# Kernel tuning notes

Measured on AMD Instinct MI355X. Metric: run time of the kernel, lower is better.

The kernel has to match this reference:

```python
import jax, jax.numpy as jnp
import numpy as np

SEQ_LEN = 4096
HIDDEN = 1280
NUM_HEADS = 16
HEAD_DIM = HIDDEN // NUM_HEADS  # 80
NUM_SEQS = 8


def setup_inputs() -> dict:
    key = jax.random.key(0)
    ks = jax.random.split(key, 8)
    x = jax.random.normal(ks[0], (SEQ_LEN, HIDDEN), dtype=jnp.float32)
    # rotary tables: use cos/sin of random angles so they are bounded like real RoPE tables
    ang = jax.random.uniform(ks[1], (SEQ_LEN, HEAD_DIM), dtype=jnp.float32) * 6.283185
    cos = jnp.cos(ang)
    sin = jnp.sin(ang)
    # variable-length packed segments: strictly increasing boundaries incl. 0 and SEQ_LEN
    rng = np.random.default_rng(0)
    inner = np.sort(rng.choice(np.arange(1, SEQ_LEN), size=NUM_SEQS - 1, replace=False))
    cu_seqlens = jnp.asarray(np.concatenate([[0], inner, [SEQ_LEN]]), dtype=jnp.int32)
    s = 0.02
    w_qkv = jax.random.normal(ks[2], (HIDDEN, 3 * HIDDEN), dtype=jnp.float32) * s
    b_qkv = jnp.zeros((3 * HIDDEN,), dtype=jnp.float32)
    w_proj = jax.random.normal(ks[3], (HIDDEN, HIDDEN), dtype=jnp.float32) * s
    b_proj = jnp.zeros((HIDDEN,), dtype=jnp.float32)
    return {"x": x, "cu_seqlens": cu_seqlens, "cos": cos, "sin": sin,
            "w_qkv": w_qkv, "b_qkv": b_qkv, "w_proj": w_proj, "b_proj": b_proj}


def _rotate_half(t):
    d = t.shape[-1] // 2
    return jnp.concatenate([-t[..., d:], t[..., :d]], axis=-1)


def _apply_rope(q, k, cos, sin):
    # q,k: (S,H,D); cos,sin: (S,D) broadcast over heads, computed in fp32
    c = cos[:, None, :].astype(jnp.float32)
    s = sin[:, None, :].astype(jnp.float32)
    qf, kf = q.astype(jnp.float32), k.astype(jnp.float32)
    q_out = qf * c + _rotate_half(qf) * s
    k_out = kf * c + _rotate_half(kf) * s
    return q_out.astype(q.dtype), k_out.astype(k.dtype)


def reference(x, cu_seqlens, cos, sin, w_qkv, b_qkv, w_proj, b_proj):
    S = x.shape[0]
    scale = HEAD_DIM ** (-0.5)
    qkv = (x @ w_qkv + b_qkv).reshape(S, 3, NUM_HEADS, HEAD_DIM)
    q, k, v = qkv[:, 0], qkv[:, 1], qkv[:, 2]  # each (S,H,D)
    q, k = _apply_rope(q, k, cos, sin)
    # block-diagonal varlen attention via segment-id mask (same math as per-chunk softmax)
    pos = jnp.arange(S)
    seg = jnp.searchsorted(cu_seqlens[1:], pos, side='right')  # (S,) segment id
    mask = seg[:, None] == seg[None, :]  # (S,S) block-diagonal
    scores = jnp.einsum('shd,thd->hst', q, k) * scale  # (H,S,S)
    scores = jnp.where(mask[None], scores.astype(jnp.float32), jnp.finfo(jnp.float32).min)
    attn = jax.nn.softmax(scores, axis=-1).astype(q.dtype)
    out = jnp.einsum('hst,thd->shd', attn, v).reshape(S, NUM_HEADS * HEAD_DIM)
    return out @ w_proj + b_proj
```

## Files before the change

### kernel.cpp

```cpp
#include <hip/hip_runtime.h>
#include <cstdint>
#include <cstddef>

typedef __bf16 bf16x8 __attribute__((ext_vector_type(8)));
typedef float f32x4 __attribute__((ext_vector_type(4)));
typedef float f32x16 __attribute__((ext_vector_type(16)));
typedef unsigned short u16x8 __attribute__((ext_vector_type(8)));

#define SEQ   4096
#define HID   1280
#define NH    16
#define HD    80

__device__ __forceinline__ unsigned short f2bf(float f) {
  unsigned int u = __float_as_uint(f);
  unsigned int r = u + 0x7FFFu + ((u >> 16) & 1u);
  return (unsigned short)(r >> 16);
}
__device__ __forceinline__ float bf2f(unsigned short h) {
  return __uint_as_float(((unsigned int)h) << 16);
}
__device__ __forceinline__ __bf16 us2bf(unsigned short u) {
  union { unsigned short s; __bf16 b; } c; c.s = u; return c.b;
}
__device__ __forceinline__ void dma16(const void* g, void* l) {
  __builtin_amdgcn_global_load_lds((const __attribute__((address_space(1))) unsigned int*)g,
                                   (__attribute__((address_space(3))) unsigned int*)l, 16, 0, 0);
}
__device__ __forceinline__ unsigned int cvtpk(float a, float b) {
  unsigned int w;
  asm("v_cvt_pk_bf16_f32 %0, %1, %2" : "=v"(w) : "v"(a), "v"(b));
  return w;
}
__device__ __forceinline__ float lo2f(unsigned int w) { return __uint_as_float(w << 16); }
__device__ __forceinline__ float hi2f(unsigned int w) { return __uint_as_float(w & 0xffff0000u); }

__global__ __launch_bounds__(256) void split_hi_kernel(const float* __restrict__ x,
                                                       unsigned short* __restrict__ hi,
                                                       int n4) {
  int i = blockIdx.x * 256 + threadIdx.x;
  if (i >= n4) return;
  float4 v = *((const float4*)x + i);
  *((ushort4*)hi + i) = make_ushort4(f2bf(v.x), f2bf(v.y), f2bf(v.z), f2bf(v.w));
}

__global__ __launch_bounds__(256) void tsplit_kernel(const float* __restrict__ W,
                                                     unsigned short* __restrict__ Thi,
                                                     unsigned short* __restrict__ Tlo,
                                                     int K, int N) {
  __shared__ float tile[32][33];
  int n0 = blockIdx.x * 32, k0 = blockIdx.y * 32;
  int tx = threadIdx.x & 31, ty = threadIdx.x >> 5;
#pragma unroll
  for (int i = 0; i < 32; i += 8)
    tile[ty + i][tx] = W[(size_t)(k0 + ty + i) * N + n0 + tx];
  __syncthreads();
#pragma unroll
  for (int i = 0; i < 32; i += 8) {
    float v = tile[tx][ty + i];
    size_t idx = (size_t)(n0 + ty + i) * K + (size_t)(k0 + tx);
    unsigned short h = f2bf(v);
    Thi[idx] = h;
    Tlo[idx] = f2bf(v - bf2f(h));
  }
}

__global__ __launch_bounds__(256, 3) void gemm128_x2(
    const unsigned short* __restrict__ A, const unsigned short* __restrict__ Bh,
    const unsigned short* __restrict__ Bl, const float* __restrict__ bias,
    float* __restrict__ out0, float* __restrict__ out1, float* __restrict__ out2,
    int M, int N, int K) {
  __shared__ __align__(16) unsigned short sALL[3 * 8192];

  const int t = threadIdx.x;
  const int lane = t & 63, wave = t >> 6;
  const int c16 = lane & 15, quad = lane >> 4;
  const int bm = blockIdx.y * 128, bn = blockIdx.x * 128;
  const int wr = (wave >> 1) * 64, wc = (wave & 1) * 64;
  const int lrow = lane >> 3;
  const int lswz = (lane & 7) ^ lrow;

  f32x4 acc[4][4];
#pragma unroll
  for (int i = 0; i < 4; ++i)
#pragma unroll
    for (int j = 0; j < 4; ++j) acc[i][j] = (f32x4){0.f, 0.f, 0.f, 0.f};

  const unsigned short* gp[12];
#pragma unroll
  for (int i = 0; i < 12; ++i) {
    const int ua = wave * 12 + i;
    const int arr = ua >> 4, sub = ua & 15;
    const unsigned short* g = (arr == 0) ? A : (arr == 1) ? Bh : Bl;
    const int rowg = ((arr == 0) ? bm : bn) + sub * 8 + lrow;
    gp[i] = g + (size_t)rowg * K + lswz * 8;
  }

  for (int k0 = 0; k0 < K; k0 += 64) {
    __syncthreads();
#pragma unroll
    for (int i = 0; i < 12; ++i)
      dma16(gp[i] + k0, &sALL[(wave * 12 + i) * 512]);
    __syncthreads();
#pragma unroll
    for (int ks = 0; ks < 2; ++ks) {
      bf16x8 a[4], bh[4], bl[4];
#pragma unroll
      for (int mi = 0; mi < 4; ++mi) {
        const int row = wr + mi * 16 + c16;
        const int off = row * 64 + (((ks * 4 + quad) ^ (row & 7)) * 8);
        a[mi] = *(const bf16x8*)&sALL[off];
      }
#pragma unroll
      for (int ni = 0; ni < 4; ++ni) {
        const int row = wc + ni * 16 + c16;
        const int off = row * 64 + (((ks * 4 + quad) ^ (row & 7)) * 8);
        bh[ni] = *(const bf16x8*)&sALL[8192 + off];
        bl[ni] = *(const bf16x8*)&sALL[16384 + off];
      }
#pragma unroll
      for (int mi = 0; mi < 4; ++mi)
#pragma unroll
        for (int ni = 0; ni < 4; ++ni) {
          acc[mi][ni] = __builtin_amdgcn_mfma_f32_16x16x32_bf16(a[mi], bh[ni], acc[mi][ni], 0, 0, 0);
          acc[mi][ni] = __builtin_amdgcn_mfma_f32_16x16x32_bf16(a[mi], bl[ni], acc[mi][ni], 0, 0, 0);
        }
    }
  }
#pragma unroll
  for (int ni = 0; ni < 4; ++ni) {
    int colg = bn + wc + ni * 16 + c16;
    float bv = bias[colg];
    float* op;
    int c = colg;
    if (c < 1280) op = out0;
    else if (c < 2560) { op = out1; c -= 1280; }
    else { op = out2; c -= 2560; }
#pragma unroll
    for (int mi = 0; mi < 4; ++mi)
#pragma unroll
      for (int r = 0; r < 4; ++r) {
        int rowg = bm + wr + mi * 16 + quad * 4 + r;
        op[(size_t)rowg * 1280 + c] = acc[mi][ni][r] + bv;
      }
  }
}

__global__ __launch_bounds__(256) void rope_pack_kernel(
    float* __restrict__ qf, const float* __restrict__ kf,
    const float* __restrict__ cs, const float* __restrict__ sn,
    unsigned short* __restrict__ khi, unsigned short* __restrict__ klo) {
  const int h = blockIdx.y;
  const int s = blockIdx.x * 64 + (threadIdx.x >> 2);
  const int p = threadIdx.x & 3;
  float* qrow = qf + (size_t)s * HID + h * HD;
  const float* krow = kf + (size_t)s * HID + h * HD;
  const float* cr = cs + (size_t)s * HD;
  const float* sr = sn + (size_t)s * HD;
  unsigned short* kh = khi + ((size_t)h * SEQ + s) * HD;
  unsigned short* kl = klo + ((size_t)h * SEQ + s) * HD;
#pragma unroll
  for (int j = 0; j < 10; ++j) {
    int d = 10 * p + j;
    float c0 = cr[d], s0 = sr[d], c1 = cr[d + 40], s1 = sr[d + 40];
    float q0 = qrow[d], q1 = qrow[d + 40];
    qrow[d]      = q0 * c0 - q1 * s0;
    qrow[d + 40] = q1 * c1 + q0 * s1;
    float k0 = krow[d], k1 = krow[d + 40];
    float kn0 = k0 * c0 - k1 * s0;
    float kn1 = k1 * c1 + k0 * s1;
    unsigned short h0 = f2bf(kn0), h1 = f2bf(kn1);
    kh[d] = h0;      kl[d] = f2bf(kn0 - bf2f(h0));
    kh[d + 40] = h1; kl[d + 40] = f2bf(kn1 - bf2f(h1));
  }
}

__global__ __launch_bounds__(256) void vt_pack_kernel(const float* __restrict__ vf,
                                                      unsigned short* __restrict__ vthi,
                                                      unsigned short* __restrict__ vtlo) {
  __shared__ unsigned short sTh[80][72];
  __shared__ unsigned short sTl[80][72];
  const int h = blockIdx.y;
  const int s0 = blockIdx.x * 64;
  const int t = threadIdx.x;
  {
    int row = t >> 2, p = (t & 3) * 20;
    const float* src = vf + (size_t)(s0 + row) * HID + h * HD + p;
#pragma unroll
    for (int i = 0; i < 5; ++i) {
      float4 v = *(const float4*)(src + 4 * i);
      float vv[4] = {v.x, v.y, v.z, v.w};
#pragma unroll
      for (int j = 0; j < 4; ++j) {
        int d = p + 4 * i + j;
        unsigned short hu = f2bf(vv[j]);
        sTh[d][row] = hu;
        sTl[d][row] = f2bf(vv[j] - bf2f(hu));
      }
    }
  }
  __syncthreads();
  if (t < 160) {
    int d = t >> 1, half = (t & 1) * 32;
    size_t base = (size_t)(h * HD + d) * SEQ + s0 + half;
#pragma unroll
    for (int i = 0; i < 8; ++i) {
      *(ushort4*)&vthi[base + 4 * i] = *(ushort4*)&sTh[d][half + 4 * i];
      *(ushort4*)&vtlo[base + 4 * i] = *(ushort4*)&sTl[d][half + 4 * i];
    }
  }
}


#define MFMA32(A, B, C) __builtin_amdgcn_mfma_f32_32x32x16_bf16(A, B, C, 0, 0, 0)

__global__ __launch_bounds__(128, 2) void attn_kernel(
    const float* __restrict__ qf, const unsigned short* __restrict__ khi,
    const unsigned short* __restrict__ klo, const unsigned short* __restrict__ vthi,
    const unsigned short* __restrict__ vtlo, const int* __restrict__ cu,
    unsigned short* __restrict__ ohi) {
  __shared__ __align__(16) unsigned short sAll[20480];
  unsigned short* const sKh = sAll;
  unsigned short* const sKl = sAll + 5120;
  unsigned short* const sVh = sAll + 10240;
  unsigned short* const sVl = sAll + 15360;

  const int t = threadIdx.x;
  const int lane = t & 63, wave = t >> 6;
  const int ln5 = lane & 31;
  const int hi  = lane >> 5;
  const int ln7 = lane & 7;
  const int lr8 = lane >> 3;
  const int vswz = (lane & 7) ^ lr8;

  const unsigned int u = (blockIdx.x & 7) * 128 + (blockIdx.x >> 3);
  const int h = (int)(u >> 6);
  const int r0 = (int)(u & 63u) * 64;

  int cu_r[9];
#pragma unroll
  for (int i = 0; i < 9; ++i) cu_r[i] = cu[i];

  const int q_my = r0 + wave * 32 + ln5;
  int sq = 0, sg0 = 0, sg1 = 0;
#pragma unroll
  for (int i = 1; i < 8; ++i) {
    sq  += (q_my    >= cu_r[i]) ? 1 : 0;
    sg0 += (r0      >= cu_r[i]) ? 1 : 0;
    sg1 += (r0 + 63 >= cu_r[i]) ? 1 : 0;
  }
  const int kb_lo = cu_r[sq], kb_hi = cu_r[sq + 1];
  const int ck0 = cu_r[sg0] & ~63;
  const int kend = cu_r[sg1 + 1];
  const int nchunk = (kend - ck0 + 63) >> 6;

  int ccol[5];
#pragma unroll
  for (int c = 0; c < 5; ++c)
    ccol[c] = (c < 4) ? ((((2 * c) + hi) ^ ln7) * 8) : ((8 + hi) * 8);

  int koff[10];
#pragma unroll
  for (int i = 0; i < 10; ++i) {
    const int G = i * 64 + lane;
    const int key = (G * 205) >> 11;
    const int p = G - key * 10;
    const int cl = (p < 8) ? (p ^ (key & 7)) : p;
    koff[i] = key * 80 + cl * 8;
  }

  const float qsc = 0.11180339887498949f;
  bf16x8 qh[5], ql[5];
  {
    const float* qrow = qf + (size_t)q_my * HID + h * HD;
#pragma unroll
    for (int kt = 0; kt < 5; ++kt) {
      const int d0 = kt * 16 + hi * 8;
      float4 a0 = *(const float4*)(qrow + d0);
      float4 a1 = *(const float4*)(qrow + d0 + 4);
      float va[8] = {a0.x, a0.y, a0.z, a0.w, a1.x, a1.y, a1.z, a1.w};
      bf16x8 hf, lf;
#pragma unroll
      for (int j = 0; j < 8; ++j) {
        float v = va[j] * qsc;
        unsigned short hu = f2bf(v);
        hf[j] = us2bf(hu);
        lf[j] = us2bf(f2bf(v - bf2f(hu)));
      }
      qh[kt] = hf; ql[kt] = lf;
    }
  }

  f32x16 O0, O1, O2;
#pragma unroll
  for (int r = 0; r < 16; ++r) { O0[r] = 0.f; O1[r] = 0.f; O2[r] = 0.f; }
  float m_i = -1e30f, l_i = 0.f;

  auto STAGE_K = [&](int ck) {
    const unsigned short* gk = (wave & 1) ? klo : khi;
    unsigned short* lk = (wave & 1) ? sKl : sKh;
    const unsigned short* gb = gk + ((size_t)h * SEQ + ck) * 80;
#pragma unroll
    for (int i2 = 0; i2 < 10; ++i2) dma16(gb + koff[i2], lk + i2 * 512);
  };
  auto STAGE_V = [&](int ck) {
    const unsigned short* gv = (wave & 1) ? vtlo : vthi;
    unsigned short* lv = (wave & 1) ? sVl : sVh;
#pragma unroll
    for (int i2 = 0; i2 < 10; ++i2)
      dma16(gv + (size_t)(h * HD + 8 * i2 + lr8) * SEQ + ck + vswz * 8, lv + i2 * 512);
  };

  STAGE_K(ck0);
  STAGE_V(ck0);
  __syncthreads();

  for (int ci = 0; ci < nchunk; ++ci) {
    const int ck = ck0 + ci * 64;

    f32x16 sc0, sc1;
#pragma unroll
    for (int r = 0; r < 16; ++r) { sc0[r] = 0.f; sc1[r] = 0.f; }
    __builtin_amdgcn_s_setprio(1);
#pragma unroll
    for (int kd = 0; kd < 5; ++kd) {
      const int col = ccol[kd];
      bf16x8 kha = *(const bf16x8*)&sKh[ln5 * 80 + col];
      bf16x8 kla = *(const bf16x8*)&sKl[ln5 * 80 + col];
      bf16x8 khb = *(const bf16x8*)&sKh[(32 + ln5) * 80 + col];
      bf16x8 klb = *(const bf16x8*)&sKl[(32 + ln5) * 80 + col];
      sc0 = MFMA32(kha, qh[kd], sc0); sc1 = MFMA32(khb, qh[kd], sc1);
      sc0 = MFMA32(kha, ql[kd], sc0); sc1 = MFMA32(khb, ql[kd], sc1);
      sc0 = MFMA32(kla, qh[kd], sc0); sc1 = MFMA32(klb, qh[kd], sc1);
    }
    __builtin_amdgcn_s_setprio(0);

    float mx = -1e30f;
#define MSK(SCV, KT2)                                                          \
    {                                                                          \
      const int kb = ck + (KT2) * 32 + 4 * hi;                                 \
      _Pragma("unroll")                                                        \
      for (int r = 0; r < 16; ++r) {                                           \
        const int kg = kb + (r & 3) + 8 * (r >> 2);                            \
        float v = (kg >= kb_lo && kg < kb_hi) ? SCV[r] : -1e30f;               \
        SCV[r] = v;                                                            \
        mx = fmaxf(mx, v);                                                     \
      }                                                                        \
    }
    MSK(sc0, 0)
    MSK(sc1, 1)
#undef MSK
    mx = fmaxf(mx, __shfl_xor(mx, 32));
    const float mnew = fmaxf(m_i, mx);
    const float alpha = __expf(m_i - mnew);
    float ps = 0.f;
#define EXPP(SCV)                                                              \
    _Pragma("unroll")                                                          \
    for (int r = 0; r < 16; ++r) {                                             \
      const float s = SCV[r];                                                  \
      const float p = (s > -1e29f) ? __expf(s - mnew) : 0.f;                   \
      ps += p;                                                                 \
      SCV[r] = p;                                                              \
    }
    EXPP(sc0)
    EXPP(sc1)
#undef EXPP
    ps += __shfl_xor(ps, 32);
    l_i = l_i * alpha + ps;
    m_i = mnew;
#pragma unroll
    for (int r = 0; r < 16; ++r) { O0[r] *= alpha; O1[r] *= alpha; O2[r] *= alpha; }

    __syncthreads();
    if (ci + 1 < nchunk) STAGE_K(ck + 64);

    __builtin_amdgcn_s_setprio(1);
#define PV_STEP(SCV, SUB, KT)                                                  \
    {                                                                          \
      unsigned int A1 = cvtpk(SCV[(SUB)*8+0], SCV[(SUB)*8+1]);                 \
      unsigned int A2 = cvtpk(SCV[(SUB)*8+2], SCV[(SUB)*8+3]);                 \
      unsigned int B1 = cvtpk(SCV[(SUB)*8+4], SCV[(SUB)*8+5]);                 \
      unsigned int B2 = cvtpk(SCV[(SUB)*8+6], SCV[(SUB)*8+7]);                 \
      float e0 = SCV[(SUB)*8+0] - lo2f(A1), e1 = SCV[(SUB)*8+1] - hi2f(A1);    \
      float e2 = SCV[(SUB)*8+2] - lo2f(A2), e3 = SCV[(SUB)*8+3] - hi2f(A2);    \
      float e4 = SCV[(SUB)*8+4] - lo2f(B1), e5 = SCV[(SUB)*8+5] - hi2f(B1);    \
      float e6 = SCV[(SUB)*8+6] - lo2f(B2), e7 = SCV[(SUB)*8+7] - hi2f(B2);    \
      unsigned int C1 = cvtpk(e0, e1), C2 = cvtpk(e2, e3);                     \
      unsigned int D1 = cvtpk(e4, e5), D2 = cvtpk(e6, e7);                     \
      unsigned int T1 = (unsigned int)__shfl_xor((int)(hi ? A1 : B1), 32);     \
      unsigned int T2 = (unsigned int)__shfl_xor((int)(hi ? A2 : B2), 32);     \
      unsigned int U1 = (unsigned int)__shfl_xor((int)(hi ? C1 : D1), 32);     \
      unsigned int U2 = (unsigned int)__shfl_xor((int)(hi ? C2 : D2), 32);     \
      union { unsigned int w[4]; bf16x8 v; } ph_, pl_;                         \
      ph_.w[0] = hi ? T1 : A1;  ph_.w[1] = hi ? T2 : A2;                       \
      ph_.w[2] = hi ? B1 : T1;  ph_.w[3] = hi ? B2 : T2;                       \
      pl_.w[0] = hi ? U1 : C1;  pl_.w[1] = hi ? U2 : C2;                       \
      pl_.w[2] = hi ? D1 : U1;  pl_.w[3] = hi ? D2 : U2;                       \
      const int vc = ccol[KT];                                                 \
      bf16x8 vh0 = *(const bf16x8*)&sVh[ln5 * 64 + vc];                        \
      bf16x8 vh1 = *(const bf16x8*)&sVh[(32 + ln5) * 64 + vc];                 \
      bf16x8 vh2 = *(const bf16x8*)&sVh[(64 + (ln5 & 15)) * 64 + vc];          \
      bf16x8 vl0 = *(const bf16x8*)&sVl[ln5 * 64 + vc];                        \
      bf16x8 vl1 = *(const bf16x8*)&sVl[(32 + ln5) * 64 + vc];                 \
      bf16x8 vl2 = *(const bf16x8*)&sVl[(64 + (ln5 & 15)) * 64 + vc];          \
      O0 = MFMA32(vh0, ph_.v, O0); O1 = MFMA32(vh1, ph_.v, O1);                \
      O2 = MFMA32(vh2, ph_.v, O2);                                             \
      O0 = MFMA32(vl0, ph_.v, O0); O1 = MFMA32(vl1, ph_.v, O1);                \
      O2 = MFMA32(vl2, ph_.v, O2);                                             \
      O0 = MFMA32(vh0, pl_.v, O0); O1 = MFMA32(vh1, pl_.v, O1);                \
      O2 = MFMA32(vh2, pl_.v, O2);                                             \
    }
    PV_STEP(sc0, 0, 0)
    PV_STEP(sc0, 1, 1)
    PV_STEP(sc1, 0, 2)
    PV_STEP(sc1, 1, 3)
#undef PV_STEP
    __builtin_amdgcn_s_setprio(0);

    __syncthreads();
    if (ci + 1 < nchunk) STAGE_V(ck + 64);
  }

  const float inv = 1.0f / l_i;
  unsigned short* tr = sAll + wave * 3072;
#define WR(OV, DT)                                                             \
  _Pragma("unroll")                                                            \
  for (int r = 0; r < 16; r += 2) {                                            \
    if ((DT) < 2 || r < 8) {                                                   \
      const int d = (DT) * 32 + (r & 3) + 8 * (r >> 2) + 4 * hi;               \
      unsigned int w = cvtpk(OV[r] * inv, OV[r + 1] * inv);                    \
      *(unsigned int*)&tr[ln5 * 96 + d] = w;                                   \
    }                                                                          \
  }
  WR(O0, 0)
  WR(O1, 1)
  WR(O2, 2)
#undef WR
  __syncthreads();
  {
    const int qq = lane >> 1, part = lane & 1;
    const unsigned short* src = tr + qq * 96 + part * 40;
    unsigned short* dst = ohi + (size_t)(r0 + wave * 32 + qq) * HID + h * HD + part * 40;
#pragma unroll
    for (int i = 0; i < 5; ++i)
      *(u16x8*)&dst[i * 8] = *(const u16x8*)&src[i * 8];
  }
}

extern "C" void kernel_launch(void* const* d_in, const int* in_sizes, int n_in,
                              void* d_out, int out_size, void* d_ws, size_t ws_size,
                              hipStream_t stream) {
  const float* x      = (const float*)d_in[0];
  const int*   cu     = (const int*)d_in[1];
  const float* cs     = (const float*)d_in[2];
  const float* sn     = (const float*)d_in[3];
  const float* w_qkv  = (const float*)d_in[4];
  const float* b_qkv  = (const float*)d_in[5];
  const float* w_proj = (const float*)d_in[6];
  const float* b_proj = (const float*)d_in[7];
  float* out = (float*)d_out;

  char* ws = (char*)d_ws;
  float*          qf     = (float*)(ws + 0);
  float*          kf     = (float*)(ws + 20971520ULL);
  unsigned short* vthi   = (unsigned short*)(ws + 20971520ULL);
  unsigned short* vtlo   = (unsigned short*)(ws + 31457280ULL);
  float*          vf     = (float*)(ws + 41943040ULL);
  unsigned short* o_hi   = (unsigned short*)(ws + 41943040ULL);
  unsigned short* x_hi   = (unsigned short*)(ws + 62914560ULL);
  unsigned short* khi    = (unsigned short*)(ws + 62914560ULL);
  unsigned short* klo    = (unsigned short*)(ws + 73400320ULL);
  unsigned short* wqt_hi = (unsigned short*)(ws + 83886080ULL);
  unsigned short* wqt_lo = (unsigned short*)(ws + 93716480ULL);
  unsigned short* wpt_hi = (unsigned short*)(ws + 103546880ULL);
  unsigned short* wpt_lo = (unsigned short*)(ws + 106823680ULL);

  split_hi_kernel<<<5120, 256, 0, stream>>>(x, x_hi, 1310720);
  tsplit_kernel<<<dim3(120, 40), 256, 0, stream>>>(w_qkv, wqt_hi, wqt_lo, 1280, 3840);
  tsplit_kernel<<<dim3(40, 40), 256, 0, stream>>>(w_proj, wpt_hi, wpt_lo, 1280, 1280);
  gemm128_x2<<<dim3(30, 32), 256, 0, stream>>>(x_hi, wqt_hi, wqt_lo, b_qkv,
                                               qf, kf, vf, 4096, 3840, 1280);
  rope_pack_kernel<<<dim3(64, 16), 256, 0, stream>>>(qf, kf, cs, sn, khi, klo);
  vt_pack_kernel<<<dim3(64, 16), 256, 0, stream>>>(vf, vthi, vtlo);
  attn_kernel<<<1024, 128, 0, stream>>>(qf, khi, klo, vthi, vtlo, cu, o_hi);
  gemm128_x2<<<dim3(10, 32), 256, 0, stream>>>(o_hi, wpt_hi, wpt_lo, b_proj,
                                               out, nullptr, nullptr, 4096, 1280, 1280);
}
```

Baseline: 369.0 us.

## Persistent per-wave attention with longest-first work queue and 32-key chunks

The attention kernel becomes persistent. Each wave independently pulls 32-query tiles from an atomic counter, in an order computed by a new single-block scheduler that sorts tiles by key-chunk count, longest first. Each wave gets its own LDS buffers and streams 32-key chunks using vmcnt-based waits instead of block-wide barriers. Scores are pre-scaled by log2(e) so exp2f replaces __expf, and the output is written straight from registers without the LDS transpose. The aim is to cut load imbalance from the varlen segments and the barrier stalls, at the cost of an extra kernel launch, atomics, and smaller MFMA tiles per chunk.

```diff
diff --git a/kernel.cpp b/kernel.cpp
--- a/kernel.cpp
+++ b/kernel.cpp
@@ -5,7 +5,6 @@
 typedef __bf16 bf16x8 __attribute__((ext_vector_type(8)));
 typedef float f32x4 __attribute__((ext_vector_type(4)));
 typedef float f32x16 __attribute__((ext_vector_type(16)));
-typedef unsigned short u16x8 __attribute__((ext_vector_type(8)));
 
 #define SEQ   4096
 #define HID   1280
@@ -211,6 +210,35 @@
   }
 }
 
+__global__ __launch_bounds__(128) void sched_kernel(const int* __restrict__ cu,
+                                                    int* __restrict__ perm,
+                                                    unsigned int* __restrict__ ctr) {
+  __shared__ int w[128];
+  const int t = threadIdx.x;
+  if (t == 0) *ctr = 0u;
+  int cu_r[9];
+#pragma unroll
+  for (int i = 0; i < 9; ++i) cu_r[i] = cu[i];
+  const int r0 = t * 32;
+  int sg0 = 0, sg1 = 0;
+#pragma unroll
+  for (int i = 1; i < 8; ++i) {
+    sg0 += (r0      >= cu_r[i]) ? 1 : 0;
+    sg1 += (r0 + 31 >= cu_r[i]) ? 1 : 0;
+  }
+  const int ck0 = cu_r[sg0] & ~31;
+  const int kend = cu_r[sg1 + 1];
+  w[t] = (kend - ck0 + 31) >> 5;
+  __syncthreads();
+  const int wt = w[t];
+  int rank = 0;
+  for (int i = 0; i < 128; ++i)
+    rank += ((w[i] > wt) || (w[i] == wt && i < t)) ? 1 : 0;
+#pragma unroll
+  for (int hh = 0; hh < 16; ++hh)
+    perm[rank * 16 + hh] = hh * 128 + t;
+}
+
 
 #define MFMA32(A, B, C) __builtin_amdgcn_mfma_f32_32x32x16_bf16(A, B, C, 0, 0, 0)
 
@@ -218,232 +246,252 @@
     const float* __restrict__ qf, const unsigned short* __restrict__ khi,
     const unsigned short* __restrict__ klo, const unsigned short* __restrict__ vthi,
     const unsigned short* __restrict__ vtlo, const int* __restrict__ cu,
-    unsigned short* __restrict__ ohi) {
+    unsigned short* __restrict__ ohi, const int* __restrict__ perm,
+    unsigned int* __restrict__ ctr) {
   __shared__ __align__(16) unsigned short sAll[20480];
-  unsigned short* const sKh = sAll;
-  unsigned short* const sKl = sAll + 5120;
-  unsigned short* const sVh = sAll + 10240;
-  unsigned short* const sVl = sAll + 15360;
 
   const int t = threadIdx.x;
   const int lane = t & 63, wave = t >> 6;
   const int ln5 = lane & 31;
   const int hi  = lane >> 5;
   const int ln7 = lane & 7;
-  const int lr8 = lane >> 3;
-  const int vswz = (lane & 7) ^ lr8;
-
-  const unsigned int u = (blockIdx.x & 7) * 128 + (blockIdx.x >> 3);
-  const int h = (int)(u >> 6);
-  const int r0 = (int)(u & 63u) * 64;
+
+  unsigned short* const wb  = sAll + wave * 10240;
+  unsigned short* const sKh = wb;
+  unsigned short* const sKl = wb + 2560;
+  unsigned short* const sVh = wb + 5120;
+  unsigned short* const sVl = wb + 7680;
 
   int cu_r[9];
 #pragma unroll
   for (int i = 0; i < 9; ++i) cu_r[i] = cu[i];
 
-  const int q_my = r0 + wave * 32 + ln5;
-  int sq = 0, sg0 = 0, sg1 = 0;
-#pragma unroll
-  for (int i = 1; i < 8; ++i) {
-    sq  += (q_my    >= cu_r[i]) ? 1 : 0;
-    sg0 += (r0      >= cu_r[i]) ? 1 : 0;
-    sg1 += (r0 + 63 >= cu_r[i]) ? 1 : 0;
-  }
-  const int kb_lo = cu_r[sq], kb_hi = cu_r[sq + 1];
-  const int ck0 = cu_r[sg0] & ~63;
-  const int kend = cu_r[sg1 + 1];
-  const int nchunk = (kend - ck0 + 63) >> 6;
-
-  int ccol[5];
-#pragma unroll
-  for (int c = 0; c < 5; ++c)
-    ccol[c] = (c < 4) ? ((((2 * c) + hi) ^ ln7) * 8) : ((8 + hi) * 8);
-
-  int koff[10];
-#pragma unroll
-  for (int i = 0; i < 10; ++i) {
+  int koff[5];
+#pragma unroll
+  for (int i = 0; i < 5; ++i) {
     const int G = i * 64 + lane;
     const int key = (G * 205) >> 11;
     const int p = G - key * 10;
     const int cl = (p < 8) ? (p ^ (key & 7)) : p;
     koff[i] = key * 80 + cl * 8;
   }
-
-  const float qsc = 0.11180339887498949f;
-  bf16x8 qh[5], ql[5];
-  {
-    const float* qrow = qf + (size_t)q_my * HID + h * HD;
-#pragma unroll
-    for (int kt = 0; kt < 5; ++kt) {
-      const int d0 = kt * 16 + hi * 8;
-      float4 a0 = *(const float4*)(qrow + d0);
-      float4 a1 = *(const float4*)(qrow + d0 + 4);
-      float va[8] = {a0.x, a0.y, a0.z, a0.w, a1.x, a1.y, a1.z, a1.w};
-      bf16x8 hf, lf;
-#pragma unroll
-      for (int j = 0; j < 8; ++j) {
-        float v = va[j] * qsc;
-        unsigned short hu = f2bf(v);
-        hf[j] = us2bf(hu);
-        lf[j] = us2bf(f2bf(v - bf2f(hu)));
-      }
-      qh[kt] = hf; ql[kt] = lf;
-    }
-  }
-
-  f32x16 O0, O1, O2;
-#pragma unroll
-  for (int r = 0; r < 16; ++r) { O0[r] = 0.f; O1[r] = 0.f; O2[r] = 0.f; }
-  float m_i = -1e30f, l_i = 0.f;
-
-  auto STAGE_K = [&](int ck) {
-    const unsigned short* gk = (wave & 1) ? klo : khi;
-    unsigned short* lk = (wave & 1) ? sKl : sKh;
-    const unsigned short* gb = gk + ((size_t)h * SEQ + ck) * 80;
-#pragma unroll
-    for (int i2 = 0; i2 < 10; ++i2) dma16(gb + koff[i2], lk + i2 * 512);
-  };
-  auto STAGE_V = [&](int ck) {
-    const unsigned short* gv = (wave & 1) ? vtlo : vthi;
-    unsigned short* lv = (wave & 1) ? sVl : sVh;
-#pragma unroll
-    for (int i2 = 0; i2 < 10; ++i2)
-      dma16(gv + (size_t)(h * HD + 8 * i2 + lr8) * SEQ + ck + vswz * 8, lv + i2 * 512);
-  };
-
-  STAGE_K(ck0);
-  STAGE_V(ck0);
-  __syncthreads();
-
-  for (int ci = 0; ci < nchunk; ++ci) {
-    const int ck = ck0 + ci * 64;
-
-    f32x16 sc0, sc1;
-#pragma unroll
-    for (int r = 0; r < 16; ++r) { sc0[r] = 0.f; sc1[r] = 0.f; }
-    __builtin_amdgcn_s_setprio(1);
-#pragma unroll
-    for (int kd = 0; kd < 5; ++kd) {
-      const int col = ccol[kd];
-      bf16x8 kha = *(const bf16x8*)&sKh[ln5 * 80 + col];
-      bf16x8 kla = *(const bf16x8*)&sKl[ln5 * 80 + col];
-      bf16x8 khb = *(const bf16x8*)&sKh[(32 + ln5) * 80 + col];
-      bf16x8 klb = *(const bf16x8*)&sKl[(32 + ln5) * 80 + col];
-      sc0 = MFMA32(kha, qh[kd], sc0); sc1 = MFMA32(khb, qh[kd], sc1);
-      sc0 = MFMA32(kha, ql[kd], sc0); sc1 = MFMA32(khb, ql[kd], sc1);
-      sc0 = MFMA32(kla, qh[kd], sc0); sc1 = MFMA32(klb, qh[kd], sc1);
-    }
-    __builtin_amdgcn_s_setprio(0);
-
-    float mx = -1e30f;
-#define MSK(SCV, KT2)                                                          \
-    {                                                                          \
-      const int kb = ck + (KT2) * 32 + 4 * hi;                                 \
-      _Pragma("unroll")                                                        \
-      for (int r = 0; r < 16; ++r) {                                           \
-        const int kg = kb + (r & 3) + 8 * (r >> 2);                            \
-        float v = (kg >= kb_lo && kg < kb_hi) ? SCV[r] : -1e30f;               \
-        SCV[r] = v;                                                            \
-        mx = fmaxf(mx, v);                                                     \
-      }                                                                        \
-    }
-    MSK(sc0, 0)
-    MSK(sc1, 1)
-#undef MSK
-    mx = fmaxf(mx, __shfl_xor(mx, 32));
-    const float mnew = fmaxf(m_i, mx);
-    const float alpha = __expf(m_i - mnew);
-    float ps = 0.f;
-#define EXPP(SCV)                                                              \
-    _Pragma("unroll")                                                          \
-    for (int r = 0; r < 16; ++r) {                                             \
-      const float s = SCV[r];                                                  \
-      const float p = (s > -1e29f) ? __expf(s - mnew) : 0.f;                   \
-      ps += p;                                                                 \
-      SCV[r] = p;                                                              \
-    }
-    EXPP(sc0)
-    EXPP(sc1)
-#undef EXPP
-    ps += __shfl_xor(ps, 32);
-    l_i = l_i * alpha + ps;
-    m_i = mnew;
-#pragma unroll
-    for (int r = 0; r < 16; ++r) { O0[r] *= alpha; O1[r] *= alpha; O2[r] *= alpha; }
-
-    __syncthreads();
-    if (ci + 1 < nchunk) STAGE_K(ck + 64);
-
-    __builtin_amdgcn_s_setprio(1);
-#define PV_STEP(SCV, SUB, KT)                                                  \
-    {                                                                          \
-      unsigned int A1 = cvtpk(SCV[(SUB)*8+0], SCV[(SUB)*8+1]);                 \
-      unsigned int A2 = cvtpk(SCV[(SUB)*8+2], SCV[(SUB)*8+3]);                 \
-      unsigned int B1 = cvtpk(SCV[(SUB)*8+4], SCV[(SUB)*8+5]);                 \
-      unsigned int B2 = cvtpk(SCV[(SUB)*8+6], SCV[(SUB)*8+7]);                 \
-      float e0 = SCV[(SUB)*8+0] - lo2f(A1), e1 = SCV[(SUB)*8+1] - hi2f(A1);    \
-      float e2 = SCV[(SUB)*8+2] - lo2f(A2), e3 = SCV[(SUB)*8+3] - hi2f(A2);    \
-      float e4 = SCV[(SUB)*8+4] - lo2f(B1), e5 = SCV[(SUB)*8+5] - hi2f(B1);    \
-      float e6 = SCV[(SUB)*8+6] - lo2f(B2), e7 = SCV[(SUB)*8+7] - hi2f(B2);    \
-      unsigned int C1 = cvtpk(e0, e1), C2 = cvtpk(e2, e3);                     \
-      unsigned int D1 = cvtpk(e4, e5), D2 = cvtpk(e6, e7);                     \
-      unsigned int T1 = (unsigned int)__shfl_xor((int)(hi ? A1 : B1), 32);     \
-      unsigned int T2 = (unsigned int)__shfl_xor((int)(hi ? A2 : B2), 32);     \
-      unsigned int U1 = (unsigned int)__shfl_xor((int)(hi ? C1 : D1), 32);     \
-      unsigned int U2 = (unsigned int)__shfl_xor((int)(hi ? C2 : D2), 32);     \
-      union { unsigned int w[4]; bf16x8 v; } ph_, pl_;                         \
-      ph_.w[0] = hi ? T1 : A1;  ph_.w[1] = hi ? T2 : A2;                       \
-      ph_.w[2] = hi ? B1 : T1;  ph_.w[3] = hi ? B2 : T2;                       \
-      pl_.w[0] = hi ? U1 : C1;  pl_.w[1] = hi ? U2 : C2;                       \
-      pl_.w[2] = hi ? D1 : U1;  pl_.w[3] = hi ? D2 : U2;                       \
-      const int vc = ccol[KT];                                                 \
-      bf16x8 vh0 = *(const bf16x8*)&sVh[ln5 * 64 + vc];                        \
-      bf16x8 vh1 = *(const bf16x8*)&sVh[(32 + ln5) * 64 + vc];                 \
-      bf16x8 vh2 = *(const bf16x8*)&sVh[(64 + (ln5 & 15)) * 64 + vc];          \
-      bf16x8 vl0 = *(const bf16x8*)&sVl[ln5 * 64 + vc];                        \
-      bf16x8 vl1 = *(const bf16x8*)&sVl[(32 + ln5) * 64 + vc];                 \
-      bf16x8 vl2 = *(const bf16x8*)&sVl[(64 + (ln5 & 15)) * 64 + vc];          \
-      O0 = MFMA32(vh0, ph_.v, O0); O1 = MFMA32(vh1, ph_.v, O1);                \
-      O2 = MFMA32(vh2, ph_.v, O2);                                             \
-      O0 = MFMA32(vl0, ph_.v, O0); O1 = MFMA32(vl1, ph_.v, O1);                \
-      O2 = MFMA32(vl2, ph_.v, O2);                                             \
-      O0 = MFMA32(vh0, pl_.v, O0); O1 = MFMA32(vh1, pl_.v, O1);                \
-      O2 = MFMA32(vh2, pl_.v, O2);                                             \
-    }
-    PV_STEP(sc0, 0, 0)
-    PV_STEP(sc0, 1, 1)
-    PV_STEP(sc1, 0, 2)
-    PV_STEP(sc1, 1, 3)
-#undef PV_STEP
-    __builtin_amdgcn_s_setprio(0);
-
-    __syncthreads();
-    if (ci + 1 < nchunk) STAGE_V(ck + 64);
-  }
-
-  const float inv = 1.0f / l_i;
-  unsigned short* tr = sAll + wave * 3072;
-#define WR(OV, DT)                                                             \
-  _Pragma("unroll")                                                            \
-  for (int r = 0; r < 16; r += 2) {                                            \
-    if ((DT) < 2 || r < 8) {                                                   \
-      const int d = (DT) * 32 + (r & 3) + 8 * (r >> 2) + 4 * hi;               \
-      unsigned int w = cvtpk(OV[r] * inv, OV[r + 1] * inv);                    \
-      *(unsigned int*)&tr[ln5 * 96 + d] = w;                                   \
-    }                                                                          \
-  }
-  WR(O0, 0)
-  WR(O1, 1)
-  WR(O2, 2)
-#undef WR
-  __syncthreads();
-  {
-    const int qq = lane >> 1, part = lane & 1;
-    const unsigned short* src = tr + qq * 96 + part * 40;
-    unsigned short* dst = ohi + (size_t)(r0 + wave * 32 + qq) * HID + h * HD + part * 40;
-#pragma unroll
-    for (int i = 0; i < 5; ++i)
-      *(u16x8*)&dst[i * 8] = *(const u16x8*)&src[i * 8];
+  int voff[5];
+#pragma unroll
+  for (int i = 0; i < 5; ++i) {
+    const int G = i * 64 + lane;
+    const int d = G >> 2, gc = G & 3;
+    const int g = gc ^ ((d >> 1) & 3);
+    voff[i] = d * SEQ + g * 8;
+  }
+  int ccol[5];
+#pragma unroll
+  for (int c = 0; c < 5; ++c)
+    ccol[c] = (c < 4) ? ((((2 * c) + hi) ^ ln7) * 8) : ((8 + hi) * 8);
+  int gcol[2];
+#pragma unroll
+  for (int c = 0; c < 2; ++c)
+    gcol[c] = (((2 * c) + hi) ^ ((ln5 >> 1) & 3)) * 8;
+
+  const float qsc = 0.11180339887498949f * 1.4426950408889634f;
+
+  for (;;) {
+    unsigned int idx = 0;
+    if (lane == 0) idx = atomicAdd(ctr, 1u);
+    idx = (unsigned int)__shfl((int)idx, 0);
+    if (idx >= 2048u) break;
+    const int uu = perm[idx];
+    const int h = uu >> 7;
+    const int r0 = (uu & 127) * 32;
+
+    const int q_my = r0 + ln5;
+    int sq = 0, sg0 = 0, sg1 = 0;
+#pragma unroll
+    for (int i = 1; i < 8; ++i) {
+      sq  += (q_my    >= cu_r[i]) ? 1 : 0;
+      sg0 += (r0      >= cu_r[i]) ? 1 : 0;
+      sg1 += (r0 + 31 >= cu_r[i]) ? 1 : 0;
+    }
+    const int kb_lo = cu_r[sq], kb_hi = cu_r[sq + 1];
+    const int ck0 = cu_r[sg0] & ~31;
+    const int kend = cu_r[sg1 + 1];
+    const int nchunk = (kend - ck0 + 31) >> 5;
+
+    bf16x8 qh[5], ql[5];
+    {
+      const float* qrow = qf + (size_t)q_my * HID + h * HD;
+#pragma unroll
+      for (int kt = 0; kt < 5; ++kt) {
+        const int d0 = kt * 16 + hi * 8;
+        float4 a0 = *(const float4*)(qrow + d0);
+        float4 a1 = *(const float4*)(qrow + d0 + 4);
+        float va[8] = {a0.x, a0.y, a0.z, a0.w, a1.x, a1.y, a1.z, a1.w};
+        bf16x8 hf, lf;
+#pragma unroll
+        for (int j = 0; j < 8; ++j) {
+          float v = va[j] * qsc;
+          unsigned short hu = f2bf(v);
+          hf[j] = us2bf(hu);
+          lf[j] = us2bf(f2bf(v - bf2f(hu)));
+        }
+        qh[kt] = hf; ql[kt] = lf;
+      }
+    }
+
+    f32x16 O0, O1, O2;
+#pragma unroll
+    for (int r = 0; r < 16; ++r) { O0[r] = 0.f; O1[r] = 0.f; O2[r] = 0.f; }
+    float m_i = -1e30f, l_i = 0.f;
+
+    const unsigned short* gkh = khi + (size_t)h * SEQ * 80;
+    const unsigned short* gkl = klo + (size_t)h * SEQ * 80;
+    const unsigned short* gvh = vthi + (size_t)h * HD * SEQ;
+    const unsigned short* gvl = vtlo + (size_t)h * HD * SEQ;
+
+    {
+      const size_t kb = (size_t)ck0 * 80;
+#pragma unroll
+      for (int i = 0; i < 5; ++i) dma16(gkh + kb + koff[i], sKh + i * 512);
+#pragma unroll
+      for (int i = 0; i < 5; ++i) dma16(gkl + kb + koff[i], sKl + i * 512);
+#pragma unroll
+      for (int i = 0; i < 5; ++i) dma16(gvh + ck0 + voff[i], sVh + i * 512);
+#pragma unroll
+      for (int i = 0; i < 5; ++i) dma16(gvl + ck0 + voff[i], sVl + i * 512);
+    }
+
+    for (int ci = 0; ci < nchunk; ++ci) {
+      const int ck = ck0 + ci * 32;
+      asm volatile("s_waitcnt vmcnt(10)" ::: "memory");
+
+      f32x16 sc;
+#pragma unroll
+      for (int r = 0; r < 16; ++r) sc[r] = 0.f;
+      __builtin_amdgcn_s_setprio(1);
+#pragma unroll
+      for (int kd = 0; kd < 5; ++kd) {
+        const int col = ccol[kd];
+        bf16x8 kh = *(const bf16x8*)&sKh[ln5 * 80 + col];
+        bf16x8 kl = *(const bf16x8*)&sKl[ln5 * 80 + col];
+        sc = MFMA32(kh, qh[kd], sc);
+        sc = MFMA32(kh, ql[kd], sc);
+        sc = MFMA32(kl, qh[kd], sc);
+      }
+      __builtin_amdgcn_s_setprio(0);
+
+      __builtin_amdgcn_sched_barrier(0);
+      if (ci + 1 < nchunk) {
+        const size_t kb = (size_t)(ck + 32) * 80;
+#pragma unroll
+        for (int i = 0; i < 5; ++i) dma16(gkh + kb + koff[i], sKh + i * 512);
+#pragma unroll
+        for (int i = 0; i < 5; ++i) dma16(gkl + kb + koff[i], sKl + i * 512);
+      }
+
+      float mx = -1e30f;
+      {
+        const int kb = ck + 4 * hi;
+#pragma unroll
+        for (int r = 0; r < 16; ++r) {
+          const int kg = kb + (r & 3) + 8 * (r >> 2);
+          float v = (kg >= kb_lo && kg < kb_hi) ? sc[r] : -1e30f;
+          sc[r] = v;
+          mx = fmaxf(mx, v);
+        }
+      }
+      mx = fmaxf(mx, __shfl_xor(mx, 32));
+      const float mnew = fmaxf(m_i, mx);
+      const float alpha = exp2f(m_i - mnew);
+      float ps = 0.f;
+#pragma unroll
+      for (int r = 0; r < 16; ++r) {
+        const float s = sc[r];
+        const float p = (s > -1e29f) ? exp2f(s - mnew) : 0.f;
+        ps += p;
+        sc[r] = p;
+      }
+      ps += __shfl_xor(ps, 32);
+      l_i = l_i * alpha + ps;
+      m_i = mnew;
+#pragma unroll
+      for (int r = 0; r < 16; ++r) { O0[r] *= alpha; O1[r] *= alpha; O2[r] *= alpha; }
+
+      if (ci + 1 < nchunk) {
+        asm volatile("s_waitcnt vmcnt(10)" ::: "memory");
+      } else {
+        asm volatile("s_waitcnt vmcnt(0)" ::: "memory");
+      }
+
+      __builtin_amdgcn_s_setprio(1);
+#pragma unroll
+      for (int KT = 0; KT < 2; ++KT) {
+        unsigned int A1 = cvtpk(sc[KT * 8 + 0], sc[KT * 8 + 1]);
+        unsigned int A2 = cvtpk(sc[KT * 8 + 2], sc[KT * 8 + 3]);
+        unsigned int B1 = cvtpk(sc[KT * 8 + 4], sc[KT * 8 + 5]);
+        unsigned int B2 = cvtpk(sc[KT * 8 + 6], sc[KT * 8 + 7]);
+        float e0 = sc[KT * 8 + 0] - lo2f(A1), e1 = sc[KT * 8 + 1] - hi2f(A1);
+        float e2 = sc[KT * 8 + 2] - lo2f(A2), e3 = sc[KT * 8 + 3] - hi2f(A2);
+        float e4 = sc[KT * 8 + 4] - lo2f(B1), e5 = sc[KT * 8 + 5] - hi2f(B1);
+        float e6 = sc[KT * 8 + 6] - lo2f(B2), e7 = sc[KT * 8 + 7] - hi2f(B2);
+        unsigned int C1 = cvtpk(e0, e1), C2 = cvtpk(e2, e3);
+        unsigned int D1 = cvtpk(e4, e5), D2 = cvtpk(e6, e7);
+        unsigned int T1 = (unsigned int)__shfl_xor((int)(hi ? A1 : B1), 32);
+        unsigned int T2 = (unsigned int)__shfl_xor((int)(hi ? A2 : B2), 32);
+        unsigned int U1 = (unsigned int)__shfl_xor((int)(hi ? C1 : D1), 32);
+        unsigned int U2 = (unsigned int)__shfl_xor((int)(hi ? C2 : D2), 32);
+        union { unsigned int w[4]; bf16x8 v; } ph_, pl_;
+        ph_.w[0] = hi ? T1 : A1;  ph_.w[1] = hi ? T2 : A2;
+        ph_.w[2] = hi ? B1 : T1;  ph_.w[3] = hi ? B2 : T2;
+        pl_.w[0] = hi ? U1 : C1;  pl_.w[1] = hi ? U2 : C2;
+        pl_.w[2] = hi ? D1 : U1;  pl_.w[3] = hi ? D2 : U2;
+        const int vc = gcol[KT];
+        bf16x8 vh0 = *(const bf16x8*)&sVh[ln5 * 32 + vc];
+        bf16x8 vh1 = *(const bf16x8*)&sVh[(32 + ln5) * 32 + vc];
+        bf16x8 vh2 = *(const bf16x8*)&sVh[(64 + (ln5 & 15)) * 32 + vc];
+        bf16x8 vl0 = *(const bf16x8*)&sVl[ln5 * 32 + vc];
+        bf16x8 vl1 = *(const bf16x8*)&sVl[(32 + ln5) * 32 + vc];
+        bf16x8 vl2 = *(const bf16x8*)&sVl[(64 + (ln5 & 15)) * 32 + vc];
+        O0 = MFMA32(vh0, ph_.v, O0); O1 = MFMA32(vh1, ph_.v, O1);
+        O2 = MFMA32(vh2, ph_.v, O2);
+        O0 = MFMA32(vl0, ph_.v, O0); O1 = MFMA32(vl1, ph_.v, O1);
+        O2 = MFMA32(vl2, ph_.v, O2);
+        O0 = MFMA32(vh0, pl_.v, O0); O1 = MFMA32(vh1, pl_.v, O1);
+        O2 = MFMA32(vh2, pl_.v, O2);
+      }
+      __builtin_amdgcn_s_setprio(0);
+
+      __builtin_amdgcn_sched_barrier(0);
+      if (ci + 1 < nchunk) {
+        const int cn = ck + 32;
+#pragma unroll
+        for (int i = 0; i < 5; ++i) dma16(gvh + cn + voff[i], sVh + i * 512);
+#pragma unroll
+        for (int i = 0; i < 5; ++i) dma16(gvl + cn + voff[i], sVl + i * 512);
+      }
+    }
+
+    const float inv = 1.0f / l_i;
+    unsigned short* orow = ohi + (size_t)q_my * HID + h * HD + 4 * hi;
+#pragma unroll
+    for (int j = 0; j < 4; ++j) {
+      unsigned long long w =
+          (unsigned long long)cvtpk(O0[4 * j] * inv, O0[4 * j + 1] * inv) |
+          ((unsigned long long)cvtpk(O0[4 * j + 2] * inv, O0[4 * j + 3] * inv) << 32);
+      *(unsigned long long*)&orow[8 * j] = w;
+    }
+#pragma unroll
+    for (int j = 0; j < 4; ++j) {
+      unsigned long long w =
+          (unsigned long long)cvtpk(O1[4 * j] * inv, O1[4 * j + 1] * inv) |
+          ((unsigned long long)cvtpk(O1[4 * j + 2] * inv, O1[4 * j + 3] * inv) << 32);
+      *(unsigned long long*)&orow[32 + 8 * j] = w;
+    }
+#pragma unroll
+    for (int j = 0; j < 2; ++j) {
+      unsigned long long w =
+          (unsigned long long)cvtpk(O2[4 * j] * inv, O2[4 * j + 1] * inv) |
+          ((unsigned long long)cvtpk(O2[4 * j + 2] * inv, O2[4 * j + 3] * inv) << 32);
+      *(unsigned long long*)&orow[64 + 8 * j] = w;
+    }
   }
 }
 
@@ -474,6 +522,8 @@
   unsigned short* wqt_lo = (unsigned short*)(ws + 93716480ULL);
   unsigned short* wpt_hi = (unsigned short*)(ws + 103546880ULL);
   unsigned short* wpt_lo = (unsigned short*)(ws + 106823680ULL);
+  unsigned int*   ctr    = (unsigned int*)(ws + 83886080ULL);
+  int*            perm   = (int*)(ws + 83886080ULL + 64);
 
   split_hi_kernel<<<5120, 256, 0, stream>>>(x, x_hi, 1310720);
   tsplit_kernel<<<dim3(120, 40), 256, 0, stream>>>(w_qkv, wqt_hi, wqt_lo, 1280, 3840);
@@ -482,7 +532,8 @@
                                                qf, kf, vf, 4096, 3840, 1280);
   rope_pack_kernel<<<dim3(64, 16), 256, 0, stream>>>(qf, kf, cs, sn, khi, klo);
   vt_pack_kernel<<<dim3(64, 16), 256, 0, stream>>>(vf, vthi, vtlo);
-  attn_kernel<<<1024, 128, 0, stream>>>(qf, khi, klo, vthi, vtlo, cu, o_hi);
+  sched_kernel<<<1, 128, 0, stream>>>(cu, perm, ctr);
+  attn_kernel<<<768, 128, 0, stream>>>(qf, khi, klo, vthi, vtlo, cu, o_hi, perm, ctr);
   gemm128_x2<<<dim3(10, 32), 256, 0, stream>>>(o_hi, wpt_hi, wpt_lo, b_proj,
                                                out, nullptr, nullptr, 4096, 1280, 1280);
 }
```

Measured after the change: 402.0 us. +8.9%, slower.
